# Kernel optimization log

Hardware: AMD Instinct MI355X
Metric: run time of the kernel (lower is better)

Reference implementation:

```python
import jax, jax.numpy as jnp
import numpy as np

N = 50000      # nodes
E = 800000     # edges
F_IN = 128     # n_features
H = 4          # n_heads
C1 = 64        # n_hidden (per-head out of layer 1)
C2 = 32        # n_classes (per-head out of layer 2)
NEG_SLOPE = 0.2
EPS = 1e-16


def setup_inputs() -> dict:
    key = jax.random.key(0)
    ks = jax.random.split(key, 12)
    x = jax.random.normal(ks[0], (N, F_IN), dtype=jnp.float32)
    edge_index = jax.random.randint(ks[1], (2, E), 0, N, dtype=jnp.int64)
    # layer 1 params (GATConv: shared lin for src/dst, att_src/att_dst vectors, bias)
    W1 = jax.random.normal(ks[2], (F_IN, H * C1), dtype=jnp.float32) * (1.0 / np.sqrt(F_IN))
    att_src1 = jax.random.normal(ks[3], (H, C1), dtype=jnp.float32) * 0.1
    att_dst1 = jax.random.normal(ks[4], (H, C1), dtype=jnp.float32) * 0.1
    b1 = jnp.zeros((C1,), dtype=jnp.float32)
    # layer 2 params
    W2 = jax.random.normal(ks[5], (C1, H * C2), dtype=jnp.float32) * (1.0 / np.sqrt(C1))
    att_src2 = jax.random.normal(ks[6], (H, C2), dtype=jnp.float32) * 0.1
    att_dst2 = jax.random.normal(ks[7], (H, C2), dtype=jnp.float32) * 0.1
    b2 = jnp.zeros((C2,), dtype=jnp.float32)
    return {"x": x, "edge_index": edge_index,
            "W1": W1, "att_src1": att_src1, "att_dst1": att_dst1, "b1": b1,
            "W2": W2, "att_src2": att_src2, "att_dst2": att_dst2, "b2": b2}


def gat_conv(x, src, dst, W, att_src, att_dst, b, heads, out_ch):
    """PyG GATConv with concat=False (head-averaged output)."""
    n = x.shape[0]
    h = (x @ W).reshape(n, heads, out_ch)                 # [N, H, C]
    a_s = jnp.einsum('nhc,hc->nh', h, att_src)            # [N, H]
    a_d = jnp.einsum('nhc,hc->nh', h, att_dst)            # [N, H]
    e = jax.nn.leaky_relu(a_s[src] + a_d[dst], NEG_SLOPE)  # [E, H]
    # segment softmax over edges grouped by destination node
    m = jax.ops.segment_max(e, dst, num_segments=n)        # [N, H]
    m = jnp.where(jnp.isfinite(m), m, 0.0)
    ex = jnp.exp(e - m[dst])                               # [E, H]
    denom = jax.ops.segment_sum(ex, dst, num_segments=n)   # [N, H]
    alpha = ex / (denom[dst] + EPS)                        # [E, H]
    # scatter-add aggregation of attended source features
    msg = alpha[:, :, None] * h[src]                       # [E, H, C]
    out = jax.ops.segment_sum(msg, dst, num_segments=n)    # [N, H, C]
    return out.mean(axis=1) + b                            # [N, C]


def reference(x, edge_index, W1, att_src1, att_dst1, b1, W2, att_src2, att_dst2, b2):
    src, dst = edge_index[0], edge_index[1]
    h = jax.nn.relu(gat_conv(x, src, dst, W1, att_src1, att_dst1, b1, H, C1))
    # dropout is identity in eval mode
    out = gat_conv(h, src, dst, W2, att_src2, att_dst2, b2, H, C2)
    return out
```

## Files before the change

### kernel.cpp

```cpp
#include <hip/hip_runtime.h>
#include <hip/hip_fp16.h>
#include <cstdint>
#include <cstddef>

#define N_NODES 50000
#define N_EDGES 800000
#define F_IN 128
#define H_HEADS 4
#define C1 64
#define C2 32
#define NEG_SLOPE 0.2f
#define EPS_GAT 1e-16f
#define SLOT_CAP 96

typedef _Float16 half8 __attribute__((ext_vector_type(8)));
typedef float f32x4 __attribute__((ext_vector_type(4)));

template<int K, int M, int Hn, int C, typename InT, bool FILL>
__global__ __launch_bounds__(256) void gemm_att_kernel(
        const InT* __restrict__ X, const float* __restrict__ W,
        _Float16* __restrict__ Hout,
        const float* __restrict__ atts, const float* __restrict__ attd,
        float* __restrict__ as_, float* __restrict__ ad_, int Nr,
        const int* __restrict__ esrc, const int* __restrict__ edst,
        int* __restrict__ cursor, unsigned short* __restrict__ slots) {
    constexpr int LDK = K + 8;
    constexpr int NCT = M / 64;
    constexpr int HPB = 64 / C;
    __shared__ _Float16 Ah[64 * LDK];
    __shared__ _Float16 Bt[64 * LDK];
    __shared__ _Float16 Ht[64 * 72];
    const int row0 = blockIdx.x * 64;
    const int t = threadIdx.x;
    const int wv = t >> 6;
    const int lane = t & 63;
    const int quad = lane >> 4;
    const int n16 = lane & 15;

    if constexpr (FILL) {
        const int gsz = gridDim.x * 256;
        for (int e = blockIdx.x * 256 + t; e < N_EDGES; e += gsz) {
            int d = edst[e];
            int p = atomicAdd(&cursor[d], 1);
            if (p < SLOT_CAP) slots[d * SLOT_CAP + p] = (unsigned short)esrc[e];
        }
    }

    if constexpr (sizeof(InT) == 4) {
        constexpr int KQ = K / 4;
#pragma unroll
        for (int j = 0; j < (64 * KQ) / 256; ++j) {
            int flat = t + 256 * j;
            int r = flat / KQ, kq = flat % KQ;
            int rg = row0 + r;
            float4 v = make_float4(0.f, 0.f, 0.f, 0.f);
            if (rg < Nr) v = *(const float4*)&X[(size_t)rg * K + 4 * kq];
            _Float16 tmp[4] = {(_Float16)v.x, (_Float16)v.y, (_Float16)v.z, (_Float16)v.w};
            *(uint2*)&Ah[r * LDK + 4 * kq] = *(const uint2*)tmp;
        }
    } else {
        constexpr int KQ = K / 8;
#pragma unroll
        for (int j = 0; j < (64 * KQ) / 256; ++j) {
            int flat = t + 256 * j;
            int r = flat / KQ, kq = flat % KQ;
            int rg = row0 + r;
            uint4 v = make_uint4(0u, 0u, 0u, 0u);
            if (rg < Nr) v = *(const uint4*)&X[(size_t)rg * K + 8 * kq];
            *(uint4*)&Ah[r * LDK + 8 * kq] = v;
        }
    }
    __syncthreads();

    half8 af[K / 32];
    const _Float16* Ap = &Ah[(16 * wv + n16) * LDK + 8 * quad];
#pragma unroll
    for (int ki = 0; ki < K / 32; ++ki) af[ki] = *(const half8*)(Ap + 32 * ki);

    for (int ct = 0; ct < NCT; ++ct) {
        const int col0 = 64 * ct;
        __syncthreads();
#pragma unroll
        for (int j = 0; j < K / 4; ++j) {
            int c = t & 63;
            int k = (t >> 6) + 4 * j;
            Bt[c * LDK + k] = (_Float16)W[(size_t)k * M + col0 + c];
        }
        __syncthreads();

        f32x4 acc[4];
#pragma unroll
        for (int nf = 0; nf < 4; ++nf) acc[nf] = (f32x4){0.f, 0.f, 0.f, 0.f};
#pragma unroll
        for (int ki = 0; ki < K / 32; ++ki) {
#pragma unroll
            for (int nf = 0; nf < 4; ++nf) {
                half8 bf = *(const half8*)&Bt[(16 * nf + n16) * LDK + 32 * ki + 8 * quad];
                acc[nf] = __builtin_amdgcn_mfma_f32_16x16x32_f16(af[ki], bf, acc[nf], 0, 0, 0);
            }
        }

        float dps[HPB][4], dpd[HPB][4];
#pragma unroll
        for (int u = 0; u < HPB; ++u)
#pragma unroll
            for (int r = 0; r < 4; ++r) { dps[u][r] = 0.f; dpd[u][r] = 0.f; }
#pragma unroll
        for (int nf = 0; nf < 4; ++nf) {
            int gc = col0 + 16 * nf + n16;
            float cs = atts[gc], cd = attd[gc];
#pragma unroll
            for (int r = 0; r < 4; ++r) {
                float av = acc[nf][r];
                dps[(16 * nf) / C][r] += av * cs;
                dpd[(16 * nf) / C][r] += av * cd;
            }
        }
#pragma unroll
        for (int u = 0; u < HPB; ++u)
#pragma unroll
            for (int r = 0; r < 4; ++r) {
                float s = dps[u][r], d = dpd[u][r];
#pragma unroll
                for (int off = 1; off < 16; off <<= 1) {
                    s += __shfl_xor(s, off, 64);
                    d += __shfl_xor(d, off, 64);
                }
                dps[u][r] = s; dpd[u][r] = d;
            }
        if (n16 == 0) {
            const int h0 = col0 / C;
#pragma unroll
            for (int r = 0; r < 4; ++r) {
                int row = row0 + 16 * wv + 4 * quad + r;
                if (row < Nr) {
#pragma unroll
                    for (int u = 0; u < HPB; ++u) {
                        as_[row * Hn + h0 + u] = dps[u][r];
                        ad_[row * Hn + h0 + u] = dpd[u][r];
                    }
                }
            }
        }

#pragma unroll
        for (int nf = 0; nf < 4; ++nf)
#pragma unroll
            for (int r = 0; r < 4; ++r)
                Ht[(16 * wv + 4 * quad + r) * 72 + 16 * nf + n16] = (_Float16)acc[nf][r];
        __syncthreads();
#pragma unroll
        for (int j = 0; j < 2; ++j) {
            int chunk = t + 256 * j;
            int r = chunk >> 3, cc = chunk & 7;
            int row = row0 + r;
            if (row < Nr) {
                uint4 v = *(const uint4*)&Ht[r * 72 + 8 * cc];
                *(uint4*)&Hout[(size_t)row * M + col0 + 8 * cc] = v;
            }
        }
    }
}

template<int Hn, int C, bool RELU, bool OUT_F16>
__global__ __launch_bounds__(256) void gat_agg_kernel(
        const int* __restrict__ degp, const unsigned short* __restrict__ slots,
        const float* __restrict__ as_, const float* __restrict__ ad_,
        const _Float16* __restrict__ Hm, const float* __restrict__ bias,
        void* __restrict__ outv, int Nr) {
    constexpr int HC = Hn * C;
    constexpr int PER = HC / 16;
    constexpr int NV = PER / 8;
    int node = blockIdx.x * 4 + (threadIdx.x >> 6);
    int lane = threadIdx.x & 63;
    if (node >= Nr) return;
    const int g = lane >> 4;
    const int l = lane & 15;
    const int h = l >> 2;
    const float ad_h = ad_[node * Hn + h];

    const int dn = min(degp[node], SLOT_CAP);
    const int begin = node * SLOT_CAP;
    const int end = begin + dn;
    const int iters = (dn + 3) >> 2;

    float acc[PER];
#pragma unroll
    for (int t = 0; t < PER; ++t) acc[t] = 0.f;
    float wsum = 0.f;

    int idx = begin + g;
    int s_cur = (idx < end) ? (int)slots[idx] : -1;
    int s_nx = (idx + 4 < end) ? (int)slots[idx + 4] : -1;
    float a_cur = 0.f;
    uint4 u_cur[NV] = {};
    if (s_cur >= 0) {
        a_cur = as_[s_cur * Hn + h];
        const uint4* hp = (const uint4*)(Hm + (size_t)s_cur * HC + l * PER);
        u_cur[0] = hp[0];
        if constexpr (NV == 2) u_cur[1] = hp[1];
    }

    for (int it = 0; it < iters; ++it) {
        const int s_pf = s_nx;
        s_nx = (idx + 8 < end) ? (int)slots[idx + 8] : -1;
        float a_nx = 0.f;
        uint4 u_nx[NV] = {};
        if (s_pf >= 0) {
            a_nx = as_[s_pf * Hn + h];
            const uint4* hp = (const uint4*)(Hm + (size_t)s_pf * HC + l * PER);
            u_nx[0] = hp[0];
            if constexpr (NV == 2) u_nx[1] = hp[1];
        }
        float logit = a_cur + ad_h;
        logit = (logit > 0.f) ? logit : NEG_SLOPE * logit;
        float w = (s_cur >= 0) ? __expf(logit) : 0.f;
        wsum += w;
#pragma unroll
        for (int v = 0; v < NV; ++v) {
            float2 f;
            f = __half22float2(*(const __half2*)&u_cur[v].x);
            acc[8 * v + 0] += w * f.x; acc[8 * v + 1] += w * f.y;
            f = __half22float2(*(const __half2*)&u_cur[v].y);
            acc[8 * v + 2] += w * f.x; acc[8 * v + 3] += w * f.y;
            f = __half22float2(*(const __half2*)&u_cur[v].z);
            acc[8 * v + 4] += w * f.x; acc[8 * v + 5] += w * f.y;
            f = __half22float2(*(const __half2*)&u_cur[v].w);
            acc[8 * v + 6] += w * f.x; acc[8 * v + 7] += w * f.y;
        }
        s_cur = s_pf; a_cur = a_nx;
#pragma unroll
        for (int v = 0; v < NV; ++v) u_cur[v] = u_nx[v];
        idx += 4;
    }

#pragma unroll
    for (int t = 0; t < PER; ++t) {
        acc[t] += __shfl_xor(acc[t], 16, 64);
        acc[t] += __shfl_xor(acc[t], 32, 64);
    }
    wsum += __shfl_xor(wsum, 16, 64);
    wsum += __shfl_xor(wsum, 32, 64);
    const float inv = 1.f / (wsum + EPS_GAT);
    float val[PER];
#pragma unroll
    for (int t = 0; t < PER; ++t) {
        float v = acc[t] * inv;
        v += __shfl_xor(v, 4, 64);
        v += __shfl_xor(v, 8, 64);
        val[t] = v * (1.0f / Hn);
    }
    if (lane < 4) {
        const int c0 = lane * PER;
#pragma unroll
        for (int t = 0; t < PER; ++t) {
            float v = val[t] + bias[c0 + t];
            if (RELU) v = fmaxf(v, 0.f);
            val[t] = v;
        }
        if constexpr (OUT_F16) {
            _Float16* o = (_Float16*)outv;
            _Float16 tmp[PER];
#pragma unroll
            for (int t = 0; t < PER; ++t) tmp[t] = (_Float16)val[t];
            uint4* d4 = (uint4*)&o[(size_t)node * C + c0];
            d4[0] = *(const uint4*)&tmp[0];
            if constexpr (NV == 2) d4[1] = *(const uint4*)&tmp[8];
        } else {
            float* o = (float*)outv;
#pragma unroll
            for (int t4 = 0; t4 < PER / 4; ++t4)
                *(float4*)&o[(size_t)node * C + c0 + 4 * t4] =
                    make_float4(val[4 * t4 + 0], val[4 * t4 + 1],
                                val[4 * t4 + 2], val[4 * t4 + 3]);
        }
    }
}

extern "C" void kernel_launch(void* const* d_in, const int* in_sizes, int n_in,
                              void* d_out, int out_size, void* d_ws, size_t ws_size,
                              hipStream_t stream) {
    const float* x    = (const float*)d_in[0];
    const int*   ei   = (const int*)d_in[1];
    const float* W1   = (const float*)d_in[2];
    const float* as1w = (const float*)d_in[3];
    const float* ad1w = (const float*)d_in[4];
    const float* b1   = (const float*)d_in[5];
    const float* W2   = (const float*)d_in[6];
    const float* as2w = (const float*)d_in[7];
    const float* ad2w = (const float*)d_in[8];
    const float* b2   = (const float*)d_in[9];
    float* out = (float*)d_out;

    const int* src = ei;
    const int* dst = ei + N_EDGES;

    char* ws = (char*)d_ws;
    size_t off = 0;
    auto alloc = [&](size_t bytes) -> void* {
        void* p = ws + off;
        off = (off + bytes + 255) & ~(size_t)255;
        return p;
    };
    int*   cursor = (int*)alloc((size_t)N_NODES * 4);
    float* as1_ = (float*)alloc((size_t)N_NODES * H_HEADS * 4);
    float* ad1_ = (float*)alloc((size_t)N_NODES * H_HEADS * 4);
    float* as2_ = (float*)alloc((size_t)N_NODES * H_HEADS * 4);
    float* ad2_ = (float*)alloc((size_t)N_NODES * H_HEADS * 4);
    _Float16* h1   = (_Float16*)alloc((size_t)N_NODES * H_HEADS * C1 * 2);
    _Float16* out1 = (_Float16*)alloc((size_t)N_NODES * C1 * 2);
    _Float16* h2   = (_Float16*)alloc((size_t)N_NODES * H_HEADS * C2 * 2);
    unsigned short* slots = (unsigned short*)alloc((size_t)N_NODES * SLOT_CAP * 2);

    hipMemsetAsync(cursor, 0, (size_t)N_NODES * 4, stream);

    gemm_att_kernel<F_IN, H_HEADS * C1, H_HEADS, C1, float, true>
        <<<(N_NODES + 63) / 64, 256, 0, stream>>>(
            x, W1, h1, as1w, ad1w, as1_, ad1_, N_NODES,
            src, dst, cursor, slots);

    gat_agg_kernel<H_HEADS, C1, true, true><<<(N_NODES + 3) / 4, 256, 0, stream>>>(
        cursor, slots, as1_, ad1_, h1, b1, (void*)out1, N_NODES);

    gemm_att_kernel<C1, H_HEADS * C2, H_HEADS, C2, _Float16, false>
        <<<(N_NODES + 63) / 64, 256, 0, stream>>>(
            out1, W2, h2, as2w, ad2w, as2_, ad2_, N_NODES,
            nullptr, nullptr, nullptr, nullptr);

    gat_agg_kernel<H_HEADS, C2, false, false><<<(N_NODES + 3) / 4, 256, 0, stream>>>(
        cursor, slots, as2_, ad2_, h2, b2, (void*)out, N_NODES);
}
```

Baseline: 281.0 us.

## Split edge slot fill into dst-partitioned kernel and pre-transpose weights to fp16

Moves the CSR-like slot fill out of the first GEMM into its own kernel, where 8 groups of blocks each handle one destination-node range, so atomics and slot writes stay in a localized region. The same kernel also transposes W1/W2 once into fp16 column-major buffers. The GEMM then loads its B tile with 16-byte vector loads instead of strided scalar float loads with per-element conversion. Each edge list is read 8 times and an extra launch is added, but per-block weight traffic drops and the GEMM no longer stalls on atomics.

```diff
diff --git a/kernel.cpp b/kernel.cpp
--- a/kernel.cpp
+++ b/kernel.cpp
@@ -12,18 +12,63 @@
 #define NEG_SLOPE 0.2f
 #define EPS_GAT 1e-16f
 #define SLOT_CAP 96
+#define FILL_BPG 64
+#define NODES_PER_GROUP 6250
 
 typedef _Float16 half8 __attribute__((ext_vector_type(8)));
 typedef float f32x4 __attribute__((ext_vector_type(4)));
 
-template<int K, int M, int Hn, int C, typename InT, bool FILL>
+template<int K, int M>
+__device__ __forceinline__ void wtrans_dev(const float* __restrict__ W,
+                                           _Float16* __restrict__ Wt,
+                                           _Float16* tile, int bm, int bk) {
+    const int m0 = bm * 64, k0 = bk * 64;
+    const int t = threadIdx.x;
+    const int c = t & 63;
+#pragma unroll
+    for (int j = 0; j < 16; ++j) {
+        int r = (t >> 6) + 4 * j;
+        tile[c * 66 + r] = (_Float16)W[(size_t)(k0 + r) * M + m0 + c];
+    }
+    __syncthreads();
+#pragma unroll
+    for (int j = 0; j < 16; ++j) {
+        int m_l = (t >> 6) + 4 * j;
+        Wt[(size_t)(m0 + m_l) * K + k0 + c] = tile[m_l * 66 + c];
+    }
+}
+
+__global__ __launch_bounds__(256) void fill_wtrans_kernel(
+        const int* __restrict__ src, const int* __restrict__ dst,
+        int* __restrict__ cursor, unsigned short* __restrict__ slots,
+        const float* __restrict__ W1, _Float16* __restrict__ wt1,
+        const float* __restrict__ W2, _Float16* __restrict__ wt2) {
+    __shared__ _Float16 tile[64 * 66];
+    const int b = blockIdx.x;
+    if (b < 8) {
+        wtrans_dev<F_IN, H_HEADS * C1>(W1, wt1, tile, b & 3, b >> 2);
+    } else if (b < 10) {
+        wtrans_dev<C1, H_HEADS * C2>(W2, wt2, tile, b - 8, 0);
+    }
+    const int g = b & 7;
+    const int bg = b >> 3;
+    const int dlo = g * NODES_PER_GROUP;
+    const int dhi = dlo + NODES_PER_GROUP;
+    for (int e = bg * 256 + (int)threadIdx.x; e < N_EDGES; e += FILL_BPG * 256) {
+        int d = dst[e];
+        if (d >= dlo && d < dhi) {
+            int p = atomicAdd(&cursor[d], 1);
+            if (p < SLOT_CAP) slots[(size_t)d * SLOT_CAP + p] = (unsigned short)src[e];
+        }
+    }
+}
+
+template<int K, int M, int Hn, int C, typename InT>
 __global__ __launch_bounds__(256) void gemm_att_kernel(
-        const InT* __restrict__ X, const float* __restrict__ W,
+        const InT* __restrict__ X, const _Float16* __restrict__ Wt,
         _Float16* __restrict__ Hout,
         const float* __restrict__ atts, const float* __restrict__ attd,
-        float* __restrict__ as_, float* __restrict__ ad_, int Nr,
-        const int* __restrict__ esrc, const int* __restrict__ edst,
-        int* __restrict__ cursor, unsigned short* __restrict__ slots) {
+        float* __restrict__ as_, float* __restrict__ ad_, int Nr) {
     constexpr int LDK = K + 8;
     constexpr int NCT = M / 64;
     constexpr int HPB = 64 / C;
@@ -37,15 +82,6 @@
     const int quad = lane >> 4;
     const int n16 = lane & 15;
 
-    if constexpr (FILL) {
-        const int gsz = gridDim.x * 256;
-        for (int e = blockIdx.x * 256 + t; e < N_EDGES; e += gsz) {
-            int d = edst[e];
-            int p = atomicAdd(&cursor[d], 1);
-            if (p < SLOT_CAP) slots[d * SLOT_CAP + p] = (unsigned short)esrc[e];
-        }
-    }
-
     if constexpr (sizeof(InT) == 4) {
         constexpr int KQ = K / 4;
 #pragma unroll
@@ -80,11 +116,15 @@
     for (int ct = 0; ct < NCT; ++ct) {
         const int col0 = 64 * ct;
         __syncthreads();
-#pragma unroll
-        for (int j = 0; j < K / 4; ++j) {
-            int c = t & 63;
-            int k = (t >> 6) + 4 * j;
-            Bt[c * LDK + k] = (_Float16)W[(size_t)k * M + col0 + c];
+        {
+            constexpr int KQ8 = K / 8;
+#pragma unroll
+            for (int j = 0; j < (64 * KQ8) / 256; ++j) {
+                int flat = t + 256 * j;
+                int c = flat / KQ8, kq = flat % KQ8;
+                uint4 v = *(const uint4*)&Wt[(size_t)(col0 + c) * K + 8 * kq];
+                *(uint4*)&Bt[c * LDK + 8 * kq] = v;
+            }
         }
         __syncthreads();
 
@@ -310,22 +350,25 @@
     _Float16* h1   = (_Float16*)alloc((size_t)N_NODES * H_HEADS * C1 * 2);
     _Float16* out1 = (_Float16*)alloc((size_t)N_NODES * C1 * 2);
     _Float16* h2   = (_Float16*)alloc((size_t)N_NODES * H_HEADS * C2 * 2);
+    _Float16* wt1  = (_Float16*)alloc((size_t)(H_HEADS * C1) * F_IN * 2);
+    _Float16* wt2  = (_Float16*)alloc((size_t)(H_HEADS * C2) * C1 * 2);
     unsigned short* slots = (unsigned short*)alloc((size_t)N_NODES * SLOT_CAP * 2);
 
     hipMemsetAsync(cursor, 0, (size_t)N_NODES * 4, stream);
 
-    gemm_att_kernel<F_IN, H_HEADS * C1, H_HEADS, C1, float, true>
+    fill_wtrans_kernel<<<8 * FILL_BPG, 256, 0, stream>>>(
+        src, dst, cursor, slots, W1, wt1, W2, wt2);
+
+    gemm_att_kernel<F_IN, H_HEADS * C1, H_HEADS, C1, float>
         <<<(N_NODES + 63) / 64, 256, 0, stream>>>(
-            x, W1, h1, as1w, ad1w, as1_, ad1_, N_NODES,
-            src, dst, cursor, slots);
+            x, wt1, h1, as1w, ad1w, as1_, ad1_, N_NODES);
 
     gat_agg_kernel<H_HEADS, C1, true, true><<<(N_NODES + 3) / 4, 256, 0, stream>>>(
         cursor, slots, as1_, ad1_, h1, b1, (void*)out1, N_NODES);
 
-    gemm_att_kernel<C1, H_HEADS * C2, H_HEADS, C2, _Float16, false>
+    gemm_att_kernel<C1, H_HEADS * C2, H_HEADS, C2, _Float16>
         <<<(N_NODES + 63) / 64, 256, 0, stream>>>(
-            out1, W2, h2, as2w, ad2w, as2_, ad2_, N_NODES,
-            nullptr, nullptr, nullptr, nullptr);
+            out1, wt2, h2, as2w, ad2w, as2_, ad2_, N_NODES);
 
     gat_agg_kernel<H_HEADS, C2, false, false><<<(N_NODES + 3) / 4, 256, 0, stream>>>(
         cursor, slots, as2_, ad2_, h2, b2, (void*)out, N_NODES);
```

Result: faster. 263.3 us (-6.3%).
